# Kernel tuning notes

Hardware: AMD Instinct MI355X
Metric: run time of the kernel (lower is better)

The kernel has to match this reference:

```python
import jax, jax.numpy as jnp
import numpy as np

M, K, N = 4096, 4096, 8192

def setup_inputs() -> dict:
    key = jax.random.key(0)
    k1, k2, k3 = jax.random.split(key, 3)
    a = jax.random.randint(k1, (M, K), -128, 128, dtype=jnp.int32).astype(jnp.int8)
    b = jax.random.randint(k2, (K, N), -128, 128, dtype=jnp.int32).astype(jnp.int8)
    scale = jax.random.uniform(k3, (N,), dtype=jnp.float32, minval=0.001, maxval=0.01)
    return {"a": a, "b": b, "scale": scale}

def reference(a, b, scale):
    acc = jax.lax.dot(a, b, preferred_element_type=jnp.int32)  # [M, N] int32
    return acc.astype(jnp.float32) * scale[None, :]  # [M, N] fp32
```

## Files before the change

kernel.cpp:

```cpp
#include <hip/hip_runtime.h>
#include <cstdint>
#include <cstddef>

#define M_DIM 4096
#define K_DIM 4096
#define N_DIM 8192
#define NKT (K_DIM / 128)

typedef int v4i __attribute__((ext_vector_type(4)));

__device__ __forceinline__ void load_lds16(const void* g, void* l) {
  __builtin_amdgcn_global_load_lds(
      (const __attribute__((address_space(1))) void*)g,
      (__attribute__((address_space(3))) void*)l,
      16, 0, 0);
}

#define FENCE() asm volatile("" ::: "memory")
#define BARRIER()                      \
  do {                                 \
    FENCE();                           \
    __builtin_amdgcn_s_barrier();      \
    FENCE();                           \
  } while (0)
#define VMCNT(n) asm volatile("s_waitcnt vmcnt(" #n ")" ::: "memory")

__device__ __forceinline__ uint32_t pack4(int4 v) {
  return ((uint32_t)v.x & 0xFFu) | (((uint32_t)v.y & 0xFFu) << 8) |
         (((uint32_t)v.z & 0xFFu) << 16) | ((uint32_t)v.w << 24);
}

__global__ __launch_bounds__(256) void pack_a_kernel(const int* __restrict__ A32,
                                                     uint8_t* __restrict__ A8) {
  const int n16 = (M_DIM * K_DIM) / 16;
  const int stride = gridDim.x * 256;
  for (int i = blockIdx.x * 256 + threadIdx.x; i < n16; i += stride) {
    const int4* src = reinterpret_cast<const int4*>(A32) + (size_t)i * 4;
    int4 o;
    o.x = (int)pack4(src[0]);
    o.y = (int)pack4(src[1]);
    o.z = (int)pack4(src[2]);
    o.w = (int)pack4(src[3]);
    reinterpret_cast<int4*>(A8)[i] = o;
  }
}

#define TPITCH 132
__global__ __launch_bounds__(256) void pack_bt_kernel(const int* __restrict__ B32,
                                                      uint8_t* __restrict__ Bt) {
  __shared__ uint8_t tile[128 * TPITCH];
  const int t = threadIdx.x;
  const int n0 = blockIdx.x * 128;
  const int k0 = blockIdx.y * 128;

#pragma unroll
  for (int c = 0; c < 16; ++c) {
    const int chunk = c * 256 + t;
    const int row = chunk >> 5;
    const int nc4 = (chunk & 31);
    const int4 v = *reinterpret_cast<const int4*>(
        B32 + (size_t)(k0 + row) * N_DIM + n0 + nc4 * 4);
    *reinterpret_cast<uint32_t*>(&tile[row * TPITCH + nc4 * 4]) = pack4(v);
  }
  __syncthreads();

  const int kc = (t & 7) << 4;
  const int nb = (t >> 3) << 2;
  uint32_t dw[16];
#pragma unroll
  for (int j = 0; j < 16; ++j)
    dw[j] = *reinterpret_cast<const uint32_t*>(&tile[(kc + j) * TPITCH + nb]);

#pragma unroll
  for (int np = 0; np < 4; ++np) {
    const uint32_t sel = (uint32_t)np | (((uint32_t)np + 4u) << 8);
    uint32_t o[4];
#pragma unroll
    for (int d = 0; d < 4; ++d) {
      const uint32_t p01 = __builtin_amdgcn_perm(dw[4 * d + 1], dw[4 * d + 0], sel);
      const uint32_t p23 = __builtin_amdgcn_perm(dw[4 * d + 3], dw[4 * d + 2], sel);
      o[d] = __builtin_amdgcn_perm(p23, p01, 0x05040100u);
    }
    const int4 v = make_int4((int)o[0], (int)o[1], (int)o[2], (int)o[3]);
    *reinterpret_cast<int4*>(Bt + (size_t)(n0 + nb + np) * K_DIM + k0 + kc) = v;
  }
}

__global__ __launch_bounds__(512, 2) void gemm_i8_kernel(
    const uint8_t* __restrict__ A, const uint8_t* __restrict__ Bt,
    const float* __restrict__ scale, float* __restrict__ C) {
  __shared__ uint8_t lds[2][2][2][128 * 128];

  const int tid = threadIdx.x;
  const int l = tid & 63;
  const int wave = tid >> 6;
  const int wr = wave >> 2;
  const int wc = wave & 3;

  int lin = blockIdx.y * (N_DIM / 256) + blockIdx.x;
  lin = (lin & 7) * 64 + (lin >> 3);
  const int bx = lin & 31;
  const int by = lin >> 5;
  const int m0 = by * 256;
  const int n0 = bx * 256;

  const int r0 = tid >> 3;
  const int r1 = (512 + tid) >> 3;
  const int s0 = tid & 7;
  const int c0 = ((s0 ^ (r0 & 7)) << 4);
  const int c1 = ((s0 ^ (r1 & 7)) << 4);
  const uint8_t* Abase = A + (size_t)m0 * K_DIM;
  const uint8_t* Bbase = Bt + (size_t)n0 * K_DIM;

#define STAGE(OP, BASE, BUF, HALF, T)                                                \
  do {                                                                               \
    load_lds16((BASE) + (size_t)((HALF)*128 + r0) * K_DIM + (T)*128 + c0,            \
               &lds[BUF][OP][HALF][tid * 16]);                                       \
    load_lds16((BASE) + (size_t)((HALF)*128 + r1) * K_DIM + (T)*128 + c1,            \
               &lds[BUF][OP][HALF][(512 + tid) * 16]);                               \
  } while (0)

  const int rb = (l & 15) * 128;
  const int aswz0 = (((0 * 4 + (l >> 4)) ^ (l & 7)) << 4);
  const int aswz1 = (((1 * 4 + (l >> 4)) ^ (l & 7)) << 4);
  const int brb = ((wc & 1) * 64) * 128;

  v4i acc[8][4];
#pragma unroll
  for (int i = 0; i < 8; ++i)
#pragma unroll
    for (int j = 0; j < 4; ++j) acc[i][j] = (v4i){0, 0, 0, 0};

  STAGE(0, Abase, 0, 0, 0);
  STAGE(0, Abase, 0, 1, 0);
  STAGE(1, Bbase, 0, 0, 0);
  STAGE(1, Bbase, 0, 1, 0);
  STAGE(1, Bbase, 1, 0, 1);
  STAGE(1, Bbase, 1, 1, 1);
  VMCNT(4);
  BARRIER();

#define MFMA_CLUSTER(MB, NB)                                                        \
  do {                                                                              \
    __builtin_amdgcn_s_setprio(1);                                                  \
    _Pragma("unroll") for (int mi = 0; mi < 4; ++mi)                                \
        _Pragma("unroll") for (int ni = 0; ni < 2; ++ni) {                          \
      acc[(MB)*4 + mi][(NB)*2 + ni] = __builtin_amdgcn_mfma_i32_16x16x64_i8(        \
          aF[mi][0], bF[(NB)*2 + ni][0], acc[(MB)*4 + mi][(NB)*2 + ni], 0, 0, 0);   \
      acc[(MB)*4 + mi][(NB)*2 + ni] = __builtin_amdgcn_mfma_i32_16x16x64_i8(        \
          aF[mi][1], bF[(NB)*2 + ni][1], acc[(MB)*4 + mi][(NB)*2 + ni], 0, 0, 0);   \
    }                                                                               \
    __builtin_amdgcn_s_setprio(0);                                                  \
    __builtin_amdgcn_sched_barrier(0);                                              \
  } while (0)

#define DO_TILE(T, BUF)                                                             \
  do {                                                                              \
    const int TA = ((T) + 1 < NKT) ? (T) + 1 : NKT - 1;     \
    const int TB = ((T) + 2 < NKT) ? (T) + 2 : NKT - 1;      \
    const uint8_t* _As = &lds[BUF][0][wr][0];                                       \
    const uint8_t* _Bs = &lds[BUF][1][wc >> 1][0];                                  \
    v4i aF[4][2];                                                                   \
    v4i bF[4][2];                                                                   \
                 \
    _Pragma("unroll") for (int mi = 0; mi < 4; ++mi) {                              \
      aF[mi][0] = *(const v4i*)&_As[mi * 2048 + rb + aswz0];                        \
      aF[mi][1] = *(const v4i*)&_As[mi * 2048 + rb + aswz1];                        \
    }                                                                               \
    _Pragma("unroll") for (int ni = 0; ni < 2; ++ni) {                              \
      bF[ni][0] = *(const v4i*)&_Bs[brb + ni * 2048 + rb + aswz0];                  \
      bF[ni][1] = *(const v4i*)&_Bs[brb + ni * 2048 + rb + aswz1];                  \
    }                                                                               \
    STAGE(0, Abase, (BUF) ^ 1, 0, TA);                                              \
    BARRIER();                                                                      \
    MFMA_CLUSTER(0, 0);                                                             \
    BARRIER();                                                                      \
                           \
    _Pragma("unroll") for (int ni = 2; ni < 4; ++ni) {                              \
      bF[ni][0] = *(const v4i*)&_Bs[brb + ni * 2048 + rb + aswz0];                  \
      bF[ni][1] = *(const v4i*)&_Bs[brb + ni * 2048 + rb + aswz1];                  \
    }                                                                               \
    STAGE(0, Abase, (BUF) ^ 1, 1, TA);                                              \
    BARRIER();                                                                      \
    MFMA_CLUSTER(0, 1);                                                             \
    BARRIER();                                                                      \
                           \
    _Pragma("unroll") for (int mi = 0; mi < 4; ++mi) {                              \
      aF[mi][0] = *(const v4i*)&_As[(4 + mi) * 2048 + rb + aswz0];                  \
      aF[mi][1] = *(const v4i*)&_As[(4 + mi) * 2048 + rb + aswz1];                  \
    }                                                                               \
    STAGE(1, Bbase, BUF, 0, TB);                                                    \
    BARRIER();                                                                      \
    MFMA_CLUSTER(1, 0);                                                             \
    BARRIER();                                                                      \
         \
    VMCNT(2);                                                                       \
    STAGE(1, Bbase, BUF, 1, TB);                                                    \
    BARRIER();                                                                      \
    MFMA_CLUSTER(1, 1);                                                             \
    BARRIER();                                                                      \
  } while (0)

  for (int t = 0; t < NKT; t += 2) {
    DO_TILE(t, 0);
    DO_TILE(t + 1, 1);
  }

  const int csub = (l >> 4) * 4;
  const int colb = n0 + wc * 64 + (l & 15);
  float* Cw = C + (size_t)(m0 + wr * 128) * N_DIM + colb;
#pragma unroll
  for (int ni = 0; ni < 4; ++ni) {
    const float s = scale[colb + ni * 16];
#pragma unroll
    for (int mi = 0; mi < 8; ++mi) {
#pragma unroll
      for (int r = 0; r < 4; ++r) {
        Cw[(size_t)(mi * 16 + csub + r) * N_DIM + ni * 16] =
            (float)acc[mi][ni][r] * s;
      }
    }
  }
#undef DO_TILE
#undef MFMA_CLUSTER
#undef STAGE
}

__global__ __launch_bounds__(256) void gemm_fallback(const int* __restrict__ A,
                                                     const int* __restrict__ B,
                                                     const float* __restrict__ scale,
                                                     float* __restrict__ C) {
  const int col = blockIdx.x * 16 + (threadIdx.x & 15);
  const int row = blockIdx.y * 16 + (threadIdx.x >> 4);
  int acc = 0;
  for (int k = 0; k < K_DIM; k += 4) {
    const int4 a = *reinterpret_cast<const int4*>(&A[(size_t)row * K_DIM + k]);
    acc += a.x * B[(size_t)(k + 0) * N_DIM + col];
    acc += a.y * B[(size_t)(k + 1) * N_DIM + col];
    acc += a.z * B[(size_t)(k + 2) * N_DIM + col];
    acc += a.w * B[(size_t)(k + 3) * N_DIM + col];
  }
  C[(size_t)row * N_DIM + col] = (float)acc * scale[col];
}

extern "C" void kernel_launch(void* const* d_in, const int* in_sizes, int n_in,
                              void* d_out, int out_size, void* d_ws, size_t ws_size,
                              hipStream_t stream) {
  const int* A32 = (const int*)d_in[0];
  const int* B32 = (const int*)d_in[1];
  const float* scale = (const float*)d_in[2];
  float* C = (float*)d_out;

  const size_t btBytes = (size_t)K_DIM * N_DIM;
  const size_t a8Bytes = (size_t)M_DIM * K_DIM;
  if (ws_size >= btBytes + a8Bytes) {
    uint8_t* Bt = (uint8_t*)d_ws;
    uint8_t* A8 = (uint8_t*)d_ws + btBytes;
    pack_a_kernel<<<2048, 256, 0, stream>>>(A32, A8);
    pack_bt_kernel<<<dim3(N_DIM / 128, K_DIM / 128), 256, 0, stream>>>(B32, Bt);
    gemm_i8_kernel<<<dim3(N_DIM / 256, M_DIM / 256), 512, 0, stream>>>(
        A8, Bt, scale, C);
  } else {
    gemm_fallback<<<dim3(N_DIM / 16, M_DIM / 16), 256, 0, stream>>>(
        A32, B32, scale, C);
  }
}
```

Baseline: 388.2 us.

## Switch int8 GEMM inner loop to 32x32x32 MFMA with reorganized fragment loads

Replaces the 16x16x64 int8 MFMA tiling with 32x32x32 int8 MFMAs, giving each wave 4x2 tiles of 16-register accumulators. All A and B LDS fragments for a K-tile are loaded up front, and an lgkmcnt wait is added before the mid-tile barrier. The epilogue is rewritten for the 32x32 output layout and uses nontemporal stores. The intent is fewer MFMA issues with more work per instruction and better LDS reuse. The cost is higher register pressure from holding all fragments, and less interleaving of LDS reads with compute.

```diff
diff --git a/kernel.cpp b/kernel.cpp
--- a/kernel.cpp
+++ b/kernel.cpp
@@ -8,6 +8,7 @@
 #define NKT (K_DIM / 128)
 
 typedef int v4i __attribute__((ext_vector_type(4)));
+typedef int v16i __attribute__((ext_vector_type(16)));
 
 __device__ __forceinline__ void load_lds16(const void* g, void* l) {
   __builtin_amdgcn_global_load_lds(
@@ -24,6 +25,7 @@
     FENCE();                           \
   } while (0)
 #define VMCNT(n) asm volatile("s_waitcnt vmcnt(" #n ")" ::: "memory")
+#define LGKM0() asm volatile("s_waitcnt lgkmcnt(0)" ::: "memory")
 
 __device__ __forceinline__ uint32_t pack4(int4 v) {
   return ((uint32_t)v.x & 0xFFu) | (((uint32_t)v.y & 0xFFu) << 8) |
@@ -120,16 +122,21 @@
                &lds[BUF][OP][HALF][(512 + tid) * 16]);                               \
   } while (0)
 
-  const int rb = (l & 15) * 128;
-  const int aswz0 = (((0 * 4 + (l >> 4)) ^ (l & 7)) << 4);
-  const int aswz1 = (((1 * 4 + (l >> 4)) ^ (l & 7)) << 4);
-  const int brb = ((wc & 1) * 64) * 128;
-
-  v4i acc[8][4];
-#pragma unroll
-  for (int i = 0; i < 8; ++i)
-#pragma unroll
-    for (int j = 0; j < 4; ++j) acc[i][j] = (v4i){0, 0, 0, 0};
+  const int l31 = l & 31;
+  const int rb = l31 * 128;
+  const int hb = l >> 5;
+  int swz[4];
+#pragma unroll
+  for (int ks = 0; ks < 4; ++ks) swz[ks] = ((ks * 2 + hb) ^ (l & 7)) << 4;
+  const int brb = (wc & 1) * 64 * 128;
+
+  v16i acc[4][2];
+#pragma unroll
+  for (int i = 0; i < 4; ++i)
+#pragma unroll
+    for (int j = 0; j < 2; ++j)
+#pragma unroll
+      for (int r = 0; r < 16; ++r) acc[i][j][r] = 0;
 
   STAGE(0, Abase, 0, 0, 0);
   STAGE(0, Abase, 0, 1, 0);
@@ -140,15 +147,13 @@
   VMCNT(4);
   BARRIER();
 
-#define MFMA_CLUSTER(MB, NB)                                                        \
+#define MFMA_Q(MB0, NB)                                                             \
   do {                                                                              \
     __builtin_amdgcn_s_setprio(1);                                                  \
-    _Pragma("unroll") for (int mi = 0; mi < 4; ++mi)                                \
-        _Pragma("unroll") for (int ni = 0; ni < 2; ++ni) {                          \
-      acc[(MB)*4 + mi][(NB)*2 + ni] = __builtin_amdgcn_mfma_i32_16x16x64_i8(        \
-          aF[mi][0], bF[(NB)*2 + ni][0], acc[(MB)*4 + mi][(NB)*2 + ni], 0, 0, 0);   \
-      acc[(MB)*4 + mi][(NB)*2 + ni] = __builtin_amdgcn_mfma_i32_16x16x64_i8(        \
-          aF[mi][1], bF[(NB)*2 + ni][1], acc[(MB)*4 + mi][(NB)*2 + ni], 0, 0, 0);   \
+    _Pragma("unroll") for (int mm = 0; mm < 2; ++mm)                                \
+        _Pragma("unroll") for (int ks = 0; ks < 4; ++ks) {                          \
+      acc[(MB0) + mm][NB] = __builtin_amdgcn_mfma_i32_32x32x32_i8(                  \
+          aF[(MB0) + mm][ks], bF[NB][ks], acc[(MB0) + mm][NB], 0, 0, 0);            \
     }                                                                               \
     __builtin_amdgcn_s_setprio(0);                                                  \
     __builtin_amdgcn_sched_barrier(0);                                              \
@@ -159,45 +164,41 @@
     const int TA = ((T) + 1 < NKT) ? (T) + 1 : NKT - 1;     \
     const int TB = ((T) + 2 < NKT) ? (T) + 2 : NKT - 1;      \
     const uint8_t* _As = &lds[BUF][0][wr][0];                                       \
-    const uint8_t* _Bs = &lds[BUF][1][wc >> 1][0];                                  \
-    v4i aF[4][2];                                                                   \
-    v4i bF[4][2];                                                                   \
+    const uint8_t* _Bs = &lds[BUF][1][wc >> 1][0];                                   \
+    v4i aF[4][4];                                                     \
+    v4i bF[2][4];                                                     \
+                                 \
+    _Pragma("unroll") for (int mb = 0; mb < 2; ++mb)                                \
+        _Pragma("unroll") for (int ks = 0; ks < 4; ++ks)                            \
+            aF[mb][ks] = *(const v4i*)&_As[mb * 4096 + rb + swz[ks]];               \
+    _Pragma("unroll") for (int ks = 0; ks < 4; ++ks)                                \
+        bF[0][ks] = *(const v4i*)&_Bs[brb + rb + swz[ks]];                          \
+    _Pragma("unroll") for (int mb = 2; mb < 4; ++mb)                                \
+        _Pragma("unroll") for (int ks = 0; ks < 4; ++ks)                            \
+            aF[mb][ks] = *(const v4i*)&_As[mb * 4096 + rb + swz[ks]];               \
+    _Pragma("unroll") for (int ks = 0; ks < 4; ++ks)                                \
+        bF[1][ks] = *(const v4i*)&_Bs[brb + 4096 + rb + swz[ks]];                   \
+                             \
+    STAGE(0, Abase, (BUF) ^ 1, 0, TA);                                              \
+    BARRIER();                                                                      \
+    MFMA_Q(0, 0);                                                                   \
+    BARRIER();                                                                      \
                  \
-    _Pragma("unroll") for (int mi = 0; mi < 4; ++mi) {                              \
-      aF[mi][0] = *(const v4i*)&_As[mi * 2048 + rb + aswz0];                        \
-      aF[mi][1] = *(const v4i*)&_As[mi * 2048 + rb + aswz1];                        \
-    }                                                                               \
-    _Pragma("unroll") for (int ni = 0; ni < 2; ++ni) {                              \
-      bF[ni][0] = *(const v4i*)&_Bs[brb + ni * 2048 + rb + aswz0];                  \
-      bF[ni][1] = *(const v4i*)&_Bs[brb + ni * 2048 + rb + aswz1];                  \
-    }                                                                               \
-    STAGE(0, Abase, (BUF) ^ 1, 0, TA);                                              \
-    BARRIER();                                                                      \
-    MFMA_CLUSTER(0, 0);                                                             \
-    BARRIER();                                                                      \
-                           \
-    _Pragma("unroll") for (int ni = 2; ni < 4; ++ni) {                              \
-      bF[ni][0] = *(const v4i*)&_Bs[brb + ni * 2048 + rb + aswz0];                  \
-      bF[ni][1] = *(const v4i*)&_Bs[brb + ni * 2048 + rb + aswz1];                  \
-    }                                                                               \
     STAGE(0, Abase, (BUF) ^ 1, 1, TA);                                              \
     BARRIER();                                                                      \
-    MFMA_CLUSTER(0, 1);                                                             \
-    BARRIER();                                                                      \
-                           \
-    _Pragma("unroll") for (int mi = 0; mi < 4; ++mi) {                              \
-      aF[mi][0] = *(const v4i*)&_As[(4 + mi) * 2048 + rb + aswz0];                  \
-      aF[mi][1] = *(const v4i*)&_As[(4 + mi) * 2048 + rb + aswz1];                  \
-    }                                                                               \
+    MFMA_Q(2, 0);                                                                   \
+    LGKM0();           \
+    BARRIER();                                                                      \
+                             \
     STAGE(1, Bbase, BUF, 0, TB);                                                    \
     BARRIER();                                                                      \
-    MFMA_CLUSTER(1, 0);                                                             \
-    BARRIER();                                                                      \
-         \
+    MFMA_Q(0, 1);                                                                   \
+    BARRIER();                                                                      \
+          \
     VMCNT(2);                                                                       \
     STAGE(1, Bbase, BUF, 1, TB);                                                    \
     BARRIER();                                                                      \
-    MFMA_CLUSTER(1, 1);                                                             \
+    MFMA_Q(2, 1);                                                                   \
     BARRIER();                                                                      \
   } while (0)
 
@@ -206,23 +207,24 @@
     DO_TILE(t + 1, 1);
   }
 
-  const int csub = (l >> 4) * 4;
-  const int colb = n0 + wc * 64 + (l & 15);
-  float* Cw = C + (size_t)(m0 + wr * 128) * N_DIM + colb;
-#pragma unroll
-  for (int ni = 0; ni < 4; ++ni) {
-    const float s = scale[colb + ni * 16];
-#pragma unroll
-    for (int mi = 0; mi < 8; ++mi) {
-#pragma unroll
-      for (int r = 0; r < 4; ++r) {
-        Cw[(size_t)(mi * 16 + csub + r) * N_DIM + ni * 16] =
-            (float)acc[mi][ni][r] * s;
+  const int colbase = n0 + wc * 64 + l31;
+  const int rowbase = m0 + wr * 128 + 4 * hb;
+#pragma unroll
+  for (int nb = 0; nb < 2; ++nb) {
+    const int col = colbase + nb * 32;
+    const float s = scale[col];
+#pragma unroll
+    for (int mb = 0; mb < 4; ++mb) {
+#pragma unroll
+      for (int r = 0; r < 16; ++r) {
+        const int row = rowbase + mb * 32 + (r & 3) + 8 * (r >> 2);
+        __builtin_nontemporal_store((float)acc[mb][nb][r] * s,
+                                    &C[(size_t)row * N_DIM + col]);
       }
     }
   }
 #undef DO_TILE
-#undef MFMA_CLUSTER
+#undef MFMA_Q
 #undef STAGE
 }
 
```

Result: slower. 454.0 us (+17.0%).
